# Kernel optimization log

Measured on AMD Instinct MI355X. Metric: run time of the kernel, lower is better.

## Reference

```python
import jax, jax.numpy as jnp
import numpy as np

B, S, D_MODEL, D_INNER = 64, 128, 1024, 1024


def setup_inputs() -> dict:
    key = jax.random.key(0)
    ks = jax.random.split(key, 10)
    sc = 0.02
    return {
        "embeddings": jax.random.normal(ks[0], (B, S, D_MODEL), dtype=jnp.float32),
        "Wq": jax.random.normal(ks[1], (D_MODEL, D_INNER), dtype=jnp.float32) * sc,
        "bq": jnp.zeros((D_INNER,), dtype=jnp.float32),
        "Wk": jax.random.normal(ks[2], (D_MODEL, D_INNER), dtype=jnp.float32) * sc,
        "bk": jnp.zeros((D_INNER,), dtype=jnp.float32),
        "Wv": jax.random.normal(ks[3], (D_MODEL, D_INNER), dtype=jnp.float32) * sc,
        "bv": jnp.zeros((D_INNER,), dtype=jnp.float32),
        "w": jax.random.normal(ks[4], (S, S), dtype=jnp.float32) * sc,
        "Wo": jax.random.normal(ks[5], (D_INNER, D_MODEL), dtype=jnp.float32) * sc,
        "bo": jnp.zeros((D_MODEL,), dtype=jnp.float32),
    }


def reference(embeddings, Wq, bq, Wk, bk, Wv, bv, w, Wo, bo):
    # embeddings: [B, S, Dm]
    seq_len = embeddings.shape[1]
    q = embeddings @ Wq + bq          # [B, S, Di]
    k = embeddings @ Wk + bk
    v = embeddings @ Wv + bv

    max_k = jnp.max(k, axis=1, keepdims=True)   # [B, 1, Di]
    exp_k = jnp.exp(k - max_k)                  # [B, S, Di]

    max_w = jnp.max(w, axis=1, keepdims=True)   # [S, 1]
    wn = w - max_w                              # [S, S]
    tril = jnp.tril(jnp.ones((seq_len, seq_len), dtype=bool))
    wn = jnp.where(tril, wn[:seq_len, :seq_len], -jnp.inf)
    # torch.einsum('bjj,bjd->bjd', exp_w, x) picks the DIAGONAL of exp_w
    # (repeated subscript j) and multiplies elementwise along the seq dim.
    diag_w = jnp.exp(jnp.diagonal(wn))          # [S]; tril diagonal is True so finite
    dw = diag_w[None, :, None]                  # [1, S, 1]

    numerator = dw * (exp_k * v)                # [B, S, Di]
    denominator = dw * exp_k                    # [B, S, Di]
    out = jax.nn.sigmoid(q) * (numerator / denominator)
    return out @ Wo + bo                        # [B, S, Dm]
```

## Files before the change

### kernel.cpp

```cpp
#include <hip/hip_runtime.h>


typedef short bf16x8 __attribute__((ext_vector_type(8)));
typedef float f32x4  __attribute__((ext_vector_type(4)));

__device__ __forceinline__ short f2bf(float f) {
  union { float f; unsigned u; } x; x.f = f;
  unsigned r = x.u + 0x7fffu + ((x.u >> 16) & 1u);
  return (short)(r >> 16);
}
__device__ __forceinline__ float bf2f(short s) {
  union { float f; unsigned u; } x; x.u = ((unsigned)(unsigned short)s) << 16;
  return x.f;
}

struct alignas(16) S8 { short v[8]; };

__global__ void cvt_bf16_kernel(const float* __restrict__ in, short* __restrict__ out, int n8) {
  int i = blockIdx.x * blockDim.x + threadIdx.x;
  if (i >= n8) return;
  const float4* p = (const float4*)in + (size_t)i * 2;
  float4 a = p[0], b = p[1];
  S8 s;
  s.v[0] = f2bf(a.x); s.v[1] = f2bf(a.y); s.v[2] = f2bf(a.z); s.v[3] = f2bf(a.w);
  s.v[4] = f2bf(b.x); s.v[5] = f2bf(b.y); s.v[6] = f2bf(b.z); s.v[7] = f2bf(b.w);
  ((S8*)out)[i] = s;
}

__global__ void transpose_cvt_kernel(const float* __restrict__ in, short* __restrict__ out,
                                     int R, int C) {
  __shared__ float tile[32][33];
  int bx = blockIdx.x * 32;
  int by = blockIdx.y * 32;
  int tx = threadIdx.x & 31, ty = threadIdx.x >> 5;
#pragma unroll
  for (int i = 0; i < 32; i += 8)
    tile[ty + i][tx] = in[(size_t)(by + ty + i) * C + bx + tx];
  __syncthreads();
#pragma unroll
  for (int i = 0; i < 32; i += 8)
    out[(size_t)(bx + ty + i) * R + by + tx] = f2bf(tile[tx][ty + i]);
}

__global__ void combine_kernel(const short* __restrict__ X2, const float* __restrict__ bq,
                               const float* __restrict__ bv, short* __restrict__ X) {
  int i = blockIdx.x * blockDim.x + threadIdx.x;
  int row = i >> 7;
  int c = (i & 127) * 8;
  S8 q8 = *(const S8*)(X2 + (size_t)row * 2048 + c);
  S8 v8 = *(const S8*)(X2 + (size_t)row * 2048 + 1024 + c);
  float4 b0 = ((const float4*)(bq + c))[0], b1 = ((const float4*)(bq + c))[1];
  float4 c0 = ((const float4*)(bv + c))[0], c1 = ((const float4*)(bv + c))[1];
  float qb[8] = {b0.x, b0.y, b0.z, b0.w, b1.x, b1.y, b1.z, b1.w};
  float vb[8] = {c0.x, c0.y, c0.z, c0.w, c1.x, c1.y, c1.z, c1.w};
  S8 o;
#pragma unroll
  for (int j = 0; j < 8; j++) {
    float q = bf2f(q8.v[j]) + qb[j];
    float v = bf2f(v8.v[j]) + vb[j];
    float s = 1.0f / (1.0f + expf(-q));
    o.v[j] = f2bf(s * v);
  }
  *(S8*)(X + (size_t)row * 1024 + c) = o;
}

#define GLDS(g, l) \
  __builtin_amdgcn_global_load_lds((const __attribute__((address_space(1))) void*)(g), \
                                   (__attribute__((address_space(3))) void*)(l), 16, 0, 0)

template <int MODE>
__global__ __launch_bounds__(256) void gemm_bt_kernel(
    const short* __restrict__ A, const short* __restrict__ BT, void* __restrict__ Cp,
    const float* __restrict__ bias, int N, int K) {
  __shared__ short As[128 * 32];
  __shared__ short Bs[128 * 32];
  const int t = threadIdx.x;
  const int lane = t & 63;
  const int w = t >> 6;
  const int bm = blockIdx.x * 128;
  const int bn = blockIdx.y * 128;
  const int wm = (w & 1) * 64;
  const int wn = (w >> 1) * 64;
  const int l16 = lane & 15;
  const int quad = lane >> 4;

  const int r0 = t >> 2;
  const int qo = (t & 3) * 8;
  const short* gA0 = A + (size_t)(bm + r0) * K + qo;
  const short* gA1 = A + (size_t)(bm + 64 + r0) * K + qo;
  const short* gB0 = BT + (size_t)(bn + r0) * K + qo;
  const short* gB1 = BT + (size_t)(bn + 64 + r0) * K + qo;
  short* lA0 = As + w * 64 * 8;
  short* lA1 = As + (256 + w * 64) * 8;
  short* lB0 = Bs + w * 64 * 8;
  short* lB1 = Bs + (256 + w * 64) * 8;

  f32x4 acc[4][4] = {};

  for (int k0 = 0; k0 < K; k0 += 32) {
    GLDS(gA0 + k0, lA0);
    GLDS(gA1 + k0, lA1);
    GLDS(gB0 + k0, lB0);
    GLDS(gB1 + k0, lB1);
    __syncthreads();

    bf16x8 av[4], bw[4];
#pragma unroll
    for (int i = 0; i < 4; i++)
      av[i] = *(const bf16x8*)(As + (wm + i * 16 + l16) * 32 + quad * 8);
#pragma unroll
    for (int j = 0; j < 4; j++)
      bw[j] = *(const bf16x8*)(Bs + (wn + j * 16 + l16) * 32 + quad * 8);
#pragma unroll
    for (int i = 0; i < 4; i++)
#pragma unroll
      for (int j = 0; j < 4; j++)
        acc[i][j] = __builtin_amdgcn_mfma_f32_16x16x32_bf16(av[i], bw[j], acc[i][j], 0, 0, 0);
    __syncthreads();
  }

#pragma unroll
  for (int i = 0; i < 4; i++)
#pragma unroll
    for (int j = 0; j < 4; j++)
#pragma unroll
      for (int r = 0; r < 4; r++) {
        int row = bm + wm + i * 16 + quad * 4 + r;
        int col = bn + wn + j * 16 + l16;
        if (MODE == 0)
          ((short*)Cp)[(size_t)row * N + col] = f2bf(acc[i][j][r]);
        else
          ((float*)Cp)[(size_t)row * N + col] = acc[i][j][r] + bias[col];
      }
}

extern "C" void kernel_launch(void* const* d_in, const int* in_sizes, int n_in,
                              void* d_out, int out_size, void* d_ws, size_t ws_size,
                              hipStream_t stream) {
  const float* emb = (const float*)d_in[0];
  const float* Wq  = (const float*)d_in[1];
  const float* bq  = (const float*)d_in[2];
  const float* Wv  = (const float*)d_in[5];
  const float* bv  = (const float*)d_in[6];
  const float* Wo  = (const float*)d_in[8];
  const float* bo  = (const float*)d_in[9];
  float* out = (float*)d_out;

  char* ws = (char*)d_ws;
  short* embB = (short*)(ws);
  short* X    = (short*)(ws);
  short* X2   = (short*)(ws + 16777216);
  short* WqvT = (short*)(ws + 50331648);
  short* WoT  = (short*)(ws + 54525952);

  cvt_bf16_kernel<<<4096, 256, 0, stream>>>(emb, embB, 1048576);
  transpose_cvt_kernel<<<dim3(32, 32), 256, 0, stream>>>(Wq, WqvT, 1024, 1024);
  transpose_cvt_kernel<<<dim3(32, 32), 256, 0, stream>>>(Wv, WqvT + 1024 * 1024, 1024, 1024);
  transpose_cvt_kernel<<<dim3(32, 32), 256, 0, stream>>>(Wo, WoT, 1024, 1024);

  gemm_bt_kernel<0><<<dim3(64, 16), 256, 0, stream>>>(embB, WqvT, (void*)X2, nullptr, 2048, 1024);
  combine_kernel<<<4096, 256, 0, stream>>>(X2, bq, bv, X);
  gemm_bt_kernel<1><<<dim3(64, 8), 256, 0, stream>>>(X, WoT, (void*)out, bo, 1024, 1024);
}
```

Measured before the change: 203.3 us.

## Fuse sigmoid-gate combine into QV GEMM epilogue and merge weight transposes

The Q and V projection GEMM now computes paired Q and V tiles for the same output columns in one block and applies bias, sigmoid and the multiply in its epilogue. This removes the intermediate bf16 X2 buffer round trip and the separate combine kernel. The three weight transpose launches are merged into a single 3D-grid launch to cut launch overhead. The epilogue uses the fast __expf, and the per-block N tile is halved for each of Q and V, which changes the data-reuse balance.

```diff
diff --git a/kernel.cpp b/kernel.cpp
--- a/kernel.cpp
+++ b/kernel.cpp
@@ -8,10 +8,6 @@
   union { float f; unsigned u; } x; x.f = f;
   unsigned r = x.u + 0x7fffu + ((x.u >> 16) & 1u);
   return (short)(r >> 16);
-}
-__device__ __forceinline__ float bf2f(short s) {
-  union { float f; unsigned u; } x; x.u = ((unsigned)(unsigned short)s) << 16;
-  return x.f;
 }
 
 struct alignas(16) S8 { short v[8]; };
@@ -27,50 +23,107 @@
   ((S8*)out)[i] = s;
 }
 
-__global__ void transpose_cvt_kernel(const float* __restrict__ in, short* __restrict__ out,
-                                     int R, int C) {
+__global__ void transpose3_kernel(const float* __restrict__ Wq, const float* __restrict__ Wv,
+                                  const float* __restrict__ Wo, short* __restrict__ WqvT,
+                                  short* __restrict__ WoT) {
+  const int RC = 1024;
+  const float* in; short* out;
+  if (blockIdx.z == 0)      { in = Wq; out = WqvT; }
+  else if (blockIdx.z == 1) { in = Wv; out = WqvT + 1024 * 1024; }
+  else                      { in = Wo; out = WoT; }
   __shared__ float tile[32][33];
   int bx = blockIdx.x * 32;
   int by = blockIdx.y * 32;
   int tx = threadIdx.x & 31, ty = threadIdx.x >> 5;
 #pragma unroll
   for (int i = 0; i < 32; i += 8)
-    tile[ty + i][tx] = in[(size_t)(by + ty + i) * C + bx + tx];
+    tile[ty + i][tx] = in[(size_t)(by + ty + i) * RC + bx + tx];
   __syncthreads();
 #pragma unroll
   for (int i = 0; i < 32; i += 8)
-    out[(size_t)(bx + ty + i) * R + by + tx] = f2bf(tile[tx][ty + i]);
-}
-
-__global__ void combine_kernel(const short* __restrict__ X2, const float* __restrict__ bq,
-                               const float* __restrict__ bv, short* __restrict__ X) {
-  int i = blockIdx.x * blockDim.x + threadIdx.x;
-  int row = i >> 7;
-  int c = (i & 127) * 8;
-  S8 q8 = *(const S8*)(X2 + (size_t)row * 2048 + c);
-  S8 v8 = *(const S8*)(X2 + (size_t)row * 2048 + 1024 + c);
-  float4 b0 = ((const float4*)(bq + c))[0], b1 = ((const float4*)(bq + c))[1];
-  float4 c0 = ((const float4*)(bv + c))[0], c1 = ((const float4*)(bv + c))[1];
-  float qb[8] = {b0.x, b0.y, b0.z, b0.w, b1.x, b1.y, b1.z, b1.w};
-  float vb[8] = {c0.x, c0.y, c0.z, c0.w, c1.x, c1.y, c1.z, c1.w};
-  S8 o;
-#pragma unroll
-  for (int j = 0; j < 8; j++) {
-    float q = bf2f(q8.v[j]) + qb[j];
-    float v = bf2f(v8.v[j]) + vb[j];
-    float s = 1.0f / (1.0f + expf(-q));
-    o.v[j] = f2bf(s * v);
-  }
-  *(S8*)(X + (size_t)row * 1024 + c) = o;
+    out[(size_t)(bx + ty + i) * RC + by + tx] = f2bf(tile[tx][ty + i]);
 }
 
 #define GLDS(g, l) \
   __builtin_amdgcn_global_load_lds((const __attribute__((address_space(1))) void*)(g), \
                                    (__attribute__((address_space(3))) void*)(l), 16, 0, 0)
 
-template <int MODE>
+__global__ __launch_bounds__(256) void gemm_qv_kernel(
+    const short* __restrict__ A, const short* __restrict__ BT,
+    const float* __restrict__ bq, const float* __restrict__ bv,
+    short* __restrict__ X, int K) {
+  __shared__ short As[128 * 32];
+  __shared__ short Bq[64 * 32];
+  __shared__ short Bv[64 * 32];
+  const int t = threadIdx.x;
+  const int lane = t & 63;
+  const int w = t >> 6;
+  const int bm = blockIdx.x * 128;
+  const int bn = blockIdx.y * 64;
+  const int wm = (w & 1) * 64;
+  const int wn = (w >> 1) * 32;
+  const int l16 = lane & 15;
+  const int quad = lane >> 4;
+
+  const int r0 = t >> 2;
+  const int qo = (t & 3) * 8;
+  const short* gA0 = A + (size_t)(bm + r0) * K + qo;
+  const short* gA1 = A + (size_t)(bm + 64 + r0) * K + qo;
+  const short* gBq = BT + (size_t)(bn + r0) * K + qo;
+  const short* gBv = BT + (size_t)(1024 + bn + r0) * K + qo;
+  short* lA0 = As + w * 512;
+  short* lA1 = As + 2048 + w * 512;
+  short* lBq = Bq + w * 512;
+  short* lBv = Bv + w * 512;
+
+  f32x4 accq[4][2] = {};
+  f32x4 accv[4][2] = {};
+
+  for (int k0 = 0; k0 < K; k0 += 32) {
+    GLDS(gA0 + k0, lA0);
+    GLDS(gA1 + k0, lA1);
+    GLDS(gBq + k0, lBq);
+    GLDS(gBv + k0, lBv);
+    __syncthreads();
+
+    bf16x8 av[4], bqf[2], bvf[2];
+#pragma unroll
+    for (int i = 0; i < 4; i++)
+      av[i] = *(const bf16x8*)(As + (wm + i * 16 + l16) * 32 + quad * 8);
+#pragma unroll
+    for (int j = 0; j < 2; j++) {
+      bqf[j] = *(const bf16x8*)(Bq + (wn + j * 16 + l16) * 32 + quad * 8);
+      bvf[j] = *(const bf16x8*)(Bv + (wn + j * 16 + l16) * 32 + quad * 8);
+    }
+#pragma unroll
+    for (int i = 0; i < 4; i++)
+#pragma unroll
+      for (int j = 0; j < 2; j++) {
+        accq[i][j] = __builtin_amdgcn_mfma_f32_16x16x32_bf16(av[i], bqf[j], accq[i][j], 0, 0, 0);
+        accv[i][j] = __builtin_amdgcn_mfma_f32_16x16x32_bf16(av[i], bvf[j], accv[i][j], 0, 0, 0);
+      }
+    __syncthreads();
+  }
+
+#pragma unroll
+  for (int j = 0; j < 2; j++) {
+    int col = bn + wn + j * 16 + l16;
+    float bql = bq[col], bvl = bv[col];
+#pragma unroll
+    for (int i = 0; i < 4; i++)
+#pragma unroll
+      for (int r = 0; r < 4; r++) {
+        int row = bm + wm + i * 16 + quad * 4 + r;
+        float q = accq[i][j][r] + bql;
+        float v = accv[i][j][r] + bvl;
+        float s = 1.0f / (1.0f + __expf(-q));
+        X[(size_t)row * 1024 + col] = f2bf(s * v);
+      }
+  }
+}
+
 __global__ __launch_bounds__(256) void gemm_bt_kernel(
-    const short* __restrict__ A, const short* __restrict__ BT, void* __restrict__ Cp,
+    const short* __restrict__ A, const short* __restrict__ BT, float* __restrict__ C,
     const float* __restrict__ bias, int N, int K) {
   __shared__ short As[128 * 32];
   __shared__ short Bs[128 * 32];
@@ -90,10 +143,10 @@
   const short* gA1 = A + (size_t)(bm + 64 + r0) * K + qo;
   const short* gB0 = BT + (size_t)(bn + r0) * K + qo;
   const short* gB1 = BT + (size_t)(bn + 64 + r0) * K + qo;
-  short* lA0 = As + w * 64 * 8;
-  short* lA1 = As + (256 + w * 64) * 8;
-  short* lB0 = Bs + w * 64 * 8;
-  short* lB1 = Bs + (256 + w * 64) * 8;
+  short* lA0 = As + w * 512;
+  short* lA1 = As + 2048 + w * 512;
+  short* lB0 = Bs + w * 512;
+  short* lB1 = Bs + 2048 + w * 512;
 
   f32x4 acc[4][4] = {};
 
@@ -120,18 +173,17 @@
   }
 
 #pragma unroll
-  for (int i = 0; i < 4; i++)
-#pragma unroll
-    for (int j = 0; j < 4; j++)
+  for (int j = 0; j < 4; j++) {
+    int col = bn + wn + j * 16 + l16;
+    float bl = bias[col];
+#pragma unroll
+    for (int i = 0; i < 4; i++)
 #pragma unroll
       for (int r = 0; r < 4; r++) {
         int row = bm + wm + i * 16 + quad * 4 + r;
-        int col = bn + wn + j * 16 + l16;
-        if (MODE == 0)
-          ((short*)Cp)[(size_t)row * N + col] = f2bf(acc[i][j][r]);
-        else
-          ((float*)Cp)[(size_t)row * N + col] = acc[i][j][r] + bias[col];
+        C[(size_t)row * N + col] = acc[i][j][r] + bl;
       }
+  }
 }
 
 extern "C" void kernel_launch(void* const* d_in, const int* in_sizes, int n_in,
@@ -148,17 +200,13 @@
 
   char* ws = (char*)d_ws;
   short* embB = (short*)(ws);
-  short* X    = (short*)(ws);
-  short* X2   = (short*)(ws + 16777216);
-  short* WqvT = (short*)(ws + 50331648);
-  short* WoT  = (short*)(ws + 54525952);
+  short* X    = (short*)(ws + 16777216);
+  short* WqvT = (short*)(ws + 33554432);
+  short* WoT  = (short*)(ws + 37748736);
 
   cvt_bf16_kernel<<<4096, 256, 0, stream>>>(emb, embB, 1048576);
-  transpose_cvt_kernel<<<dim3(32, 32), 256, 0, stream>>>(Wq, WqvT, 1024, 1024);
-  transpose_cvt_kernel<<<dim3(32, 32), 256, 0, stream>>>(Wv, WqvT + 1024 * 1024, 1024, 1024);
-  transpose_cvt_kernel<<<dim3(32, 32), 256, 0, stream>>>(Wo, WoT, 1024, 1024);
-
-  gemm_bt_kernel<0><<<dim3(64, 16), 256, 0, stream>>>(embB, WqvT, (void*)X2, nullptr, 2048, 1024);
-  combine_kernel<<<4096, 256, 0, stream>>>(X2, bq, bv, X);
-  gemm_bt_kernel<1><<<dim3(64, 8), 256, 0, stream>>>(X, WoT, (void*)out, bo, 1024, 1024);
-}
+  transpose3_kernel<<<dim3(32, 32, 3), 256, 0, stream>>>(Wq, Wv, Wo, WqvT, WoT);
+
+  gemm_qv_kernel<<<dim3(64, 16), 256, 0, stream>>>(embB, WqvT, bq, bv, X, 1024);
+  gemm_bt_kernel<<<dim3(64, 8), 256, 0, stream>>>(X, WoT, out, bo, 1024, 1024);
+}
```

New measurement: 194.8 us. 4.2% less time.
